# Kernel tuning notes

Hardware: AMD Instinct MI355X
Metric: run time of the kernel (lower is better)

## Reference

```python
import jax, jax.numpy as jnp
import numpy as np

N_NODES = 100000
N_EDGES = 1600000
D = 64
HID = 512
N_CLASSES = 393


def gcn_conv(x, src, dst, W, b):
    """PyG-style GCNConv: h = x W; add self-loops; symmetric deg^-1/2 norm; scatter-add."""
    n = x.shape[0]
    h = x @ W  # [N, out]
    loop = jnp.arange(n)
    s = jnp.concatenate([src, loop])
    d = jnp.concatenate([dst, loop])
    deg = jax.ops.segment_sum(jnp.ones(d.shape[0], dtype=h.dtype), d, num_segments=n)
    dinv = jax.lax.rsqrt(jnp.maximum(deg, 1.0))  # self-loops guarantee deg >= 1
    norm = dinv[s] * dinv[d]  # [E+N]
    msg = h[s] * norm[:, None]  # [E+N, out] gather + scale
    out = jax.ops.segment_sum(msg, d, num_segments=n)  # scatter-add
    return out + b


def setup_inputs() -> dict:
    key = jax.random.key(0)
    ks = jax.random.split(key, 10)
    sc = 1.0 / np.sqrt(D)
    inp = {
        "adj": jax.random.randint(ks[0], (2, N_EDGES), 0, N_NODES, dtype=jnp.int64),
        "features": jax.random.normal(ks[1], (N_NODES, D), dtype=jnp.float32),
        "W1": jax.random.normal(ks[2], (D, D), dtype=jnp.float32) * sc,
        "b1": jnp.zeros((D,), jnp.float32),
        "W2": jax.random.normal(ks[3], (D, D), dtype=jnp.float32) * sc,
        "b2": jnp.zeros((D,), jnp.float32),
        "W3": jax.random.normal(ks[4], (D, D), dtype=jnp.float32) * sc,
        "b3": jnp.zeros((D,), jnp.float32),
        "Wlin": jax.random.normal(ks[5], (D, D), dtype=jnp.float32) * sc,
        "blin": jnp.zeros((D,), jnp.float32),
        "W4": jax.random.normal(ks[6], (N_NODES, HID), dtype=jnp.float32) / np.sqrt(N_NODES),
        "b4": jnp.zeros((HID,), jnp.float32),
        "W5": jax.random.normal(ks[7], (HID, N_CLASSES), dtype=jnp.float32) / np.sqrt(HID),
        "b5": jnp.zeros((N_CLASSES,), jnp.float32),
    }
    return inp


def reference(adj, features, W1, b1, W2, b2, W3, b3, Wlin, blin, W4, b4, W5, b5):
    src, dst = adj[0], adj[1]
    h = jax.nn.relu(gcn_conv(features, src, dst, W1, b1))
    h = jax.nn.relu(gcn_conv(h, src, dst, W2, b2))
    h = jax.nn.relu(gcn_conv(h, src, dst, W3, b3))
    scores = h @ Wlin + blin          # [N, 64]
    scores = scores.T                 # [64, N]
    scores = jax.nn.relu(scores @ W4 + b4)  # [64, HID]
    scores = scores @ W5 + b5         # [64, n_classes]
    return jax.nn.log_softmax(scores, axis=1)
```

## Files before the change

kernel.cpp:

```cpp
#include <hip/hip_runtime.h>
#include <math.h>

#define NN 100000
#define NE 1600000
#define HID 512
#define NCLS 393

__global__ void k_init(int* __restrict__ cnt, int* __restrict__ gtot) {
    int i = blockIdx.x * 256 + threadIdx.x;
    if (i < NN) cnt[i] = 0;
    if (i == 0) *gtot = 0;
}

__global__ void k_count(const int* __restrict__ dst, int* __restrict__ cnt) {
    int e = blockIdx.x * 256 + threadIdx.x;
    if (e < NE) atomicAdd(&cnt[dst[e]], 1);
}

__global__ void k_off(const int* __restrict__ cnt, float* __restrict__ dinv,
                      int* __restrict__ off, int* __restrict__ cur, int* __restrict__ gtot) {
    int i = blockIdx.x * 256 + threadIdx.x;
    if (i < NN) {
        int c = cnt[i];
        dinv[i] = rsqrtf(1.0f + (float)c);
        off[i] = atomicAdd(gtot, c);
        cur[i] = 0;
    }
}

__global__ void k_fill(const int* __restrict__ src, const int* __restrict__ dst,
                       const float* __restrict__ dinv, const int* __restrict__ off,
                       int* __restrict__ cur, int2* __restrict__ epack) {
    int e = blockIdx.x * 256 + threadIdx.x;
    if (e < NE) {
        int s = src[e], d = dst[e];
        int pos = off[d] + atomicAdd(&cur[d], 1);
        epack[pos] = make_int2(s, __float_as_int(dinv[s] * dinv[d]));
    }
}

template<bool IN_ACT, bool OUT_BIAS>
__global__ void k_gemm64b(const float* __restrict__ x, const float* __restrict__ W,
                          const float* __restrict__ bin, const float* __restrict__ bout,
                          float* __restrict__ out) {
    __shared__ float Ws[64 * 64];
    __shared__ float xs[32 * 64];
    int tid = threadIdx.x;
    size_t n0 = (size_t)blockIdx.x * 32;
    for (int i = tid; i < 1024; i += 256)
        ((float4*)Ws)[i] = ((const float4*)W)[i];
    for (int i = tid; i < 512; i += 256) {
        float4 v = ((const float4*)(x + n0 * 64))[i];
        if (IN_ACT) {
            int c = (i & 15) * 4;
            float4 bv = *(const float4*)(bin + c);
            v.x = fmaxf(v.x + bv.x, 0.f);
            v.y = fmaxf(v.y + bv.y, 0.f);
            v.z = fmaxf(v.z + bv.z, 0.f);
            v.w = fmaxf(v.w + bv.w, 0.f);
        }
        ((float4*)xs)[i] = v;
    }
    __syncthreads();
    int j = tid & 63, q = tid >> 6;
    float Wreg[64];
#pragma unroll
    for (int k = 0; k < 64; ++k) Wreg[k] = Ws[k * 64 + j];
    float bo = OUT_BIAS ? bout[j] : 0.f;
    for (int r = 0; r < 8; ++r) {
        int row = q * 8 + r;
        float acc = bo;
        const float4* xr = (const float4*)(xs + row * 64);
#pragma unroll
        for (int k4 = 0; k4 < 16; ++k4) {
            float4 xv = xr[k4];
            acc = fmaf(xv.x, Wreg[k4 * 4 + 0], acc);
            acc = fmaf(xv.y, Wreg[k4 * 4 + 1], acc);
            acc = fmaf(xv.z, Wreg[k4 * 4 + 2], acc);
            acc = fmaf(xv.w, Wreg[k4 * 4 + 3], acc);
        }
        out[(n0 + row) * 64 + j] = acc;
    }
}

__global__ void k_gather2(const int2* __restrict__ epack, const int* __restrict__ off,
                          const int* __restrict__ cnt, const float* __restrict__ dinv,
                          const float* __restrict__ t, float* __restrict__ out) {
    int lane = threadIdx.x & 63;
    int n = (blockIdx.x * 256 + threadIdx.x) >> 6;
    if (n >= NN) return;
    int g = lane >> 4, f4 = lane & 15;
    int o = off[n], c = cnt[n];
    float ax = 0.f, ay = 0.f, az = 0.f, aw = 0.f;
    for (int b = 0; b < c; b += 4) {
        int idx = b + g;
        if (idx < c) {
            int2 ep = epack[o + idx];
            float w = __int_as_float(ep.y);
            float4 v = *(const float4*)(t + (size_t)ep.x * 64 + f4 * 4);
            ax = fmaf(v.x, w, ax);
            ay = fmaf(v.y, w, ay);
            az = fmaf(v.z, w, az);
            aw = fmaf(v.w, w, aw);
        }
    }
    ax += __shfl_xor(ax, 16); ay += __shfl_xor(ay, 16);
    az += __shfl_xor(az, 16); aw += __shfl_xor(aw, 16);
    ax += __shfl_xor(ax, 32); ay += __shfl_xor(ay, 32);
    az += __shfl_xor(az, 32); aw += __shfl_xor(aw, 32);
    if (lane < 16) {
        float dv = dinv[n];
        float d2 = dv * dv;
        float4 self = *(const float4*)(t + (size_t)n * 64 + f4 * 4);
        float4 r;
        r.x = ax + self.x * d2;
        r.y = ay + self.y * d2;
        r.z = az + self.z * d2;
        r.w = aw + self.w * d2;
        *(float4*)(out + (size_t)n * 64 + f4 * 4) = r;
    }
}

#define TG_SPLIT 192
#define TG_CHUNK 521
__global__ void k_tgemm3(const float* __restrict__ scores, const float* __restrict__ W4,
                         float* __restrict__ Pp) {
    __shared__ float ss[64 * 64];
    int colT = blockIdx.x & 3;
    int kc = blockIdx.x >> 2;
    int tid = threadIdx.x;
    int tc = tid & 31, tr = tid >> 5;
    int col = colT * 128 + tc * 4;
    float acc[8][4];
#pragma unroll
    for (int i = 0; i < 8; ++i)
#pragma unroll
        for (int c = 0; c < 4; ++c) acc[i][c] = 0.f;
    int k0 = kc * TG_CHUNK;
    int k1 = min(k0 + TG_CHUNK, NN);
    for (int kb = k0; kb < k1; kb += 64) {
        int cnt = min(64, k1 - kb);
        __syncthreads();
        for (int i = tid; i < 1024; i += 256) {
            float4 v = {0.f, 0.f, 0.f, 0.f};
            if ((i >> 4) < cnt) v = ((const float4*)(scores + (size_t)kb * 64))[i];
            ((float4*)ss)[i] = v;
        }
        __syncthreads();
        const float* w4base = W4 + (size_t)kb * 512 + col;
        for (int nIt = 0; nIt < cnt; ++nIt) {
            float4 w = *(const float4*)(w4base + (size_t)nIt * 512);
            const float4* sp = (const float4*)(ss + nIt * 64 + tr * 8);
            float4 s0 = sp[0], s1 = sp[1];
            float sa[8] = {s0.x, s0.y, s0.z, s0.w, s1.x, s1.y, s1.z, s1.w};
#pragma unroll
            for (int i = 0; i < 8; ++i) {
                acc[i][0] = fmaf(sa[i], w.x, acc[i][0]);
                acc[i][1] = fmaf(sa[i], w.y, acc[i][1]);
                acc[i][2] = fmaf(sa[i], w.z, acc[i][2]);
                acc[i][3] = fmaf(sa[i], w.w, acc[i][3]);
            }
        }
    }
    float* pb = Pp + (size_t)kc * 64 * 512;
#pragma unroll
    for (int i = 0; i < 8; ++i) {
        int row = tr * 8 + i;
        *(float4*)(pb + row * 512 + col) = make_float4(acc[i][0], acc[i][1], acc[i][2], acc[i][3]);
    }
}

__global__ void k_reduce(const float* __restrict__ Pp, float* __restrict__ P) {
    int i = blockIdx.x * 256 + threadIdx.x;
    float s0 = 0.f, s1 = 0.f, s2 = 0.f, s3 = 0.f;
    for (int kc = 0; kc < TG_SPLIT; kc += 4) {
        s0 += Pp[(size_t)(kc + 0) * 32768 + i];
        s1 += Pp[(size_t)(kc + 1) * 32768 + i];
        s2 += Pp[(size_t)(kc + 2) * 32768 + i];
        s3 += Pp[(size_t)(kc + 3) * 32768 + i];
    }
    P[i] = (s0 + s1) + (s2 + s3);
}

__global__ void k_final(const float* __restrict__ P, const float* __restrict__ b4,
                        const float* __restrict__ W5, const float* __restrict__ b5,
                        float* __restrict__ out) {
    __shared__ float p[HID];
    __shared__ float z[NCLS];
    __shared__ float red[256];
    int i = blockIdx.x;
    int tid = threadIdx.x;
    for (int k = tid; k < HID; k += 256) p[k] = fmaxf(P[i * HID + k] + b4[k], 0.f);
    __syncthreads();
    for (int c = tid; c < NCLS; c += 256) {
        float acc = b5[c];
        for (int k = 0; k < HID; ++k) acc = fmaf(p[k], W5[(size_t)k * NCLS + c], acc);
        z[c] = acc;
    }
    __syncthreads();
    float m = -INFINITY;
    for (int c = tid; c < NCLS; c += 256) m = fmaxf(m, z[c]);
    red[tid] = m;
    __syncthreads();
    for (int s = 128; s > 0; s >>= 1) {
        if (tid < s) red[tid] = fmaxf(red[tid], red[tid + s]);
        __syncthreads();
    }
    m = red[0];
    __syncthreads();
    float sum = 0.f;
    for (int c = tid; c < NCLS; c += 256) sum += expf(z[c] - m);
    red[tid] = sum;
    __syncthreads();
    for (int s = 128; s > 0; s >>= 1) {
        if (tid < s) red[tid] += red[tid + s];
        __syncthreads();
    }
    float lse = m + logf(red[0]);
    for (int c = tid; c < NCLS; c += 256) out[i * NCLS + c] = z[c] - lse;
}

extern "C" void kernel_launch(void* const* d_in, const int* in_sizes, int n_in,
                              void* d_out, int out_size, void* d_ws, size_t ws_size,
                              hipStream_t stream) {
    const int* adj = (const int*)d_in[0];
    const int* src = adj;
    const int* dst = adj + NE;
    const float* feat = (const float*)d_in[1];
    const float* W1 = (const float*)d_in[2];
    const float* b1 = (const float*)d_in[3];
    const float* W2 = (const float*)d_in[4];
    const float* b2 = (const float*)d_in[5];
    const float* W3 = (const float*)d_in[6];
    const float* b3 = (const float*)d_in[7];
    const float* Wlin = (const float*)d_in[8];
    const float* blin = (const float*)d_in[9];
    const float* W4 = (const float*)d_in[10];
    const float* b4 = (const float*)d_in[11];
    const float* W5 = (const float*)d_in[12];
    const float* b5 = (const float*)d_in[13];
    float* out = (float*)d_out;

    char* ws = (char*)d_ws;
    float* dinv  = (float*)ws;  ws += (size_t)NN * 4;
    int*   cnt   = (int*)ws;    ws += (size_t)NN * 4;
    int*   off   = (int*)ws;    ws += (size_t)NN * 4;
    int*   cur   = (int*)ws;    ws += (size_t)NN * 4;
    int*   gtot  = (int*)ws;    ws += 16;
    int2*  epack = (int2*)ws;   ws += (size_t)NE * 8;
    float* bufA  = (float*)ws;  ws += (size_t)NN * 64 * 4;
    float* bufB  = (float*)ws;  ws += (size_t)NN * 64 * 4;
    float* P     = (float*)ws;  ws += 64 * HID * 4;

    const int NB_N = (NN + 255) / 256;
    const int NB_E = NE / 256;
    const int NB_G = NN / 32;
    const int NB_GA = NN / 4;
    const int NB_T = 4 * TG_SPLIT;

    k_init<<<NB_N, 256, 0, stream>>>(cnt, gtot);
    k_count<<<NB_E, 256, 0, stream>>>(dst, cnt);
    k_off<<<NB_N, 256, 0, stream>>>(cnt, dinv, off, cur, gtot);
    k_fill<<<NB_E, 256, 0, stream>>>(src, dst, dinv, off, cur, epack);

    k_gemm64b<false, false><<<NB_G, 256, 0, stream>>>(feat, W1, nullptr, nullptr, bufA);
    k_gather2<<<NB_GA, 256, 0, stream>>>(epack, off, cnt, dinv, bufA, bufB);
    k_gemm64b<true, false><<<NB_G, 256, 0, stream>>>(bufB, W2, b1, nullptr, bufA);
    k_gather2<<<NB_GA, 256, 0, stream>>>(epack, off, cnt, dinv, bufA, bufB);
    k_gemm64b<true, false><<<NB_G, 256, 0, stream>>>(bufB, W3, b2, nullptr, bufA);
    k_gather2<<<NB_GA, 256, 0, stream>>>(epack, off, cnt, dinv, bufA, bufB);
    k_gemm64b<true, true><<<NB_G, 256, 0, stream>>>(bufB, Wlin, b3, blin, bufA);

    float* Pp = bufB;
    k_tgemm3<<<NB_T, 256, 0, stream>>>(bufA, W4, Pp);
    k_reduce<<<(64 * HID) / 256, 256, 0, stream>>>(Pp, P);

    k_final<<<64, 256, 0, stream>>>(P, b4, W5, b5, out);
}
```

Measured before the change: 958.9 us.

## Widen gather per-lane loads, rebalance tgemm split, and replace init with memset

The neighbor gather now processes 8 edges per step, with each lane loading 8 floats. It clamps indices instead of branching, so more row loads are in flight per wavefront. The big transposed GEMM uses more, shorter K chunks with fixed trip counts and batches four W4 row loads ahead. The partial sums are reduced by a block-level 4-way split. Smaller changes swap the init kernel for hipMemsetAsync, give the 64x64 GEMM two accumulators, and reorder the workspace so the larger partial buffer may overwrite the dead edge list.

```diff
diff --git a/kernel.cpp b/kernel.cpp
--- a/kernel.cpp
+++ b/kernel.cpp
@@ -5,12 +5,6 @@
 #define NE 1600000
 #define HID 512
 #define NCLS 393
-
-__global__ void k_init(int* __restrict__ cnt, int* __restrict__ gtot) {
-    int i = blockIdx.x * 256 + threadIdx.x;
-    if (i < NN) cnt[i] = 0;
-    if (i == 0) *gtot = 0;
-}
 
 __global__ void k_count(const int* __restrict__ dst, int* __restrict__ cnt) {
     int e = blockIdx.x * 256 + threadIdx.x;
@@ -69,61 +63,78 @@
     float bo = OUT_BIAS ? bout[j] : 0.f;
     for (int r = 0; r < 8; ++r) {
         int row = q * 8 + r;
-        float acc = bo;
+        float accA = bo, accB = 0.f;
         const float4* xr = (const float4*)(xs + row * 64);
 #pragma unroll
-        for (int k4 = 0; k4 < 16; ++k4) {
-            float4 xv = xr[k4];
-            acc = fmaf(xv.x, Wreg[k4 * 4 + 0], acc);
-            acc = fmaf(xv.y, Wreg[k4 * 4 + 1], acc);
-            acc = fmaf(xv.z, Wreg[k4 * 4 + 2], acc);
-            acc = fmaf(xv.w, Wreg[k4 * 4 + 3], acc);
-        }
-        out[(n0 + row) * 64 + j] = acc;
-    }
-}
-
-__global__ void k_gather2(const int2* __restrict__ epack, const int* __restrict__ off,
+        for (int k4 = 0; k4 < 16; k4 += 2) {
+            float4 x0 = xr[k4], x1 = xr[k4 + 1];
+            accA = fmaf(x0.x, Wreg[k4 * 4 + 0], accA);
+            accA = fmaf(x0.y, Wreg[k4 * 4 + 1], accA);
+            accA = fmaf(x0.z, Wreg[k4 * 4 + 2], accA);
+            accA = fmaf(x0.w, Wreg[k4 * 4 + 3], accA);
+            accB = fmaf(x1.x, Wreg[k4 * 4 + 4], accB);
+            accB = fmaf(x1.y, Wreg[k4 * 4 + 5], accB);
+            accB = fmaf(x1.z, Wreg[k4 * 4 + 6], accB);
+            accB = fmaf(x1.w, Wreg[k4 * 4 + 7], accB);
+        }
+        out[(n0 + row) * 64 + j] = accA + accB;
+    }
+}
+
+__global__ void k_gather3(const int2* __restrict__ epack, const int* __restrict__ off,
                           const int* __restrict__ cnt, const float* __restrict__ dinv,
                           const float* __restrict__ t, float* __restrict__ out) {
     int lane = threadIdx.x & 63;
     int n = (blockIdx.x * 256 + threadIdx.x) >> 6;
     if (n >= NN) return;
-    int g = lane >> 4, f4 = lane & 15;
+    int g = lane >> 3, fl = lane & 7;
     int o = off[n], c = cnt[n];
-    float ax = 0.f, ay = 0.f, az = 0.f, aw = 0.f;
-    for (int b = 0; b < c; b += 4) {
-        int idx = b + g;
-        if (idx < c) {
-            int2 ep = epack[o + idx];
-            float w = __int_as_float(ep.y);
-            float4 v = *(const float4*)(t + (size_t)ep.x * 64 + f4 * 4);
-            ax = fmaf(v.x, w, ax);
-            ay = fmaf(v.y, w, ay);
-            az = fmaf(v.z, w, az);
-            aw = fmaf(v.w, w, aw);
-        }
-    }
-    ax += __shfl_xor(ax, 16); ay += __shfl_xor(ay, 16);
-    az += __shfl_xor(az, 16); aw += __shfl_xor(aw, 16);
-    ax += __shfl_xor(ax, 32); ay += __shfl_xor(ay, 32);
-    az += __shfl_xor(az, 32); aw += __shfl_xor(aw, 32);
-    if (lane < 16) {
+    float4 a0 = {0.f, 0.f, 0.f, 0.f}, a1 = {0.f, 0.f, 0.f, 0.f};
+    if (c > 0) {
+        for (int b = 0; b < c; b += 8) {
+            int idx = b + g;
+            int2 ep = epack[o + min(idx, c - 1)];
+            float w = (idx < c) ? __int_as_float(ep.y) : 0.f;
+            const float* row = t + (size_t)ep.x * 64 + fl * 8;
+            float4 v0 = *(const float4*)row;
+            float4 v1 = *(const float4*)(row + 4);
+            a0.x = fmaf(v0.x, w, a0.x);
+            a0.y = fmaf(v0.y, w, a0.y);
+            a0.z = fmaf(v0.z, w, a0.z);
+            a0.w = fmaf(v0.w, w, a0.w);
+            a1.x = fmaf(v1.x, w, a1.x);
+            a1.y = fmaf(v1.y, w, a1.y);
+            a1.z = fmaf(v1.z, w, a1.z);
+            a1.w = fmaf(v1.w, w, a1.w);
+        }
+    }
+#pragma unroll
+    for (int m = 8; m <= 32; m <<= 1) {
+        a0.x += __shfl_xor(a0.x, m); a0.y += __shfl_xor(a0.y, m);
+        a0.z += __shfl_xor(a0.z, m); a0.w += __shfl_xor(a0.w, m);
+        a1.x += __shfl_xor(a1.x, m); a1.y += __shfl_xor(a1.y, m);
+        a1.z += __shfl_xor(a1.z, m); a1.w += __shfl_xor(a1.w, m);
+    }
+    if (lane < 8) {
         float dv = dinv[n];
         float d2 = dv * dv;
-        float4 self = *(const float4*)(t + (size_t)n * 64 + f4 * 4);
-        float4 r;
-        r.x = ax + self.x * d2;
-        r.y = ay + self.y * d2;
-        r.z = az + self.z * d2;
-        r.w = aw + self.w * d2;
-        *(float4*)(out + (size_t)n * 64 + f4 * 4) = r;
-    }
-}
-
-#define TG_SPLIT 192
-#define TG_CHUNK 521
-__global__ void k_tgemm3(const float* __restrict__ scores, const float* __restrict__ W4,
+        const float* srow = t + (size_t)n * 64 + fl * 8;
+        float4 s0 = *(const float4*)srow;
+        float4 s1 = *(const float4*)(srow + 4);
+        float4 r0, r1;
+        r0.x = a0.x + s0.x * d2; r0.y = a0.y + s0.y * d2;
+        r0.z = a0.z + s0.z * d2; r0.w = a0.w + s0.w * d2;
+        r1.x = a1.x + s1.x * d2; r1.y = a1.y + s1.y * d2;
+        r1.z = a1.z + s1.z * d2; r1.w = a1.w + s1.w * d2;
+        float* orow = out + (size_t)n * 64 + fl * 8;
+        *(float4*)orow = r0;
+        *(float4*)(orow + 4) = r1;
+    }
+}
+
+#define TG_SPLIT 261
+#define TG_CHUNK 384
+__global__ void k_tgemm4(const float* __restrict__ scores, const float* __restrict__ W4,
                          float* __restrict__ Pp) {
     __shared__ float ss[64 * 64];
     int colT = blockIdx.x & 3;
@@ -137,28 +148,34 @@
 #pragma unroll
         for (int c = 0; c < 4; ++c) acc[i][c] = 0.f;
     int k0 = kc * TG_CHUNK;
-    int k1 = min(k0 + TG_CHUNK, NN);
-    for (int kb = k0; kb < k1; kb += 64) {
-        int cnt = min(64, k1 - kb);
+    for (int st = 0; st < 6; ++st) {
+        int kb = k0 + st * 64;
         __syncthreads();
         for (int i = tid; i < 1024; i += 256) {
             float4 v = {0.f, 0.f, 0.f, 0.f};
-            if ((i >> 4) < cnt) v = ((const float4*)(scores + (size_t)kb * 64))[i];
+            if (kb + (i >> 4) < NN) v = ((const float4*)(scores + (size_t)kb * 64))[i];
             ((float4*)ss)[i] = v;
         }
         __syncthreads();
-        const float* w4base = W4 + (size_t)kb * 512 + col;
-        for (int nIt = 0; nIt < cnt; ++nIt) {
-            float4 w = *(const float4*)(w4base + (size_t)nIt * 512);
-            const float4* sp = (const float4*)(ss + nIt * 64 + tr * 8);
-            float4 s0 = sp[0], s1 = sp[1];
-            float sa[8] = {s0.x, s0.y, s0.z, s0.w, s1.x, s1.y, s1.z, s1.w};
-#pragma unroll
-            for (int i = 0; i < 8; ++i) {
-                acc[i][0] = fmaf(sa[i], w.x, acc[i][0]);
-                acc[i][1] = fmaf(sa[i], w.y, acc[i][1]);
-                acc[i][2] = fmaf(sa[i], w.z, acc[i][2]);
-                acc[i][3] = fmaf(sa[i], w.w, acc[i][3]);
+        for (int nIt = 0; nIt < 64; nIt += 4) {
+            float4 w[4];
+#pragma unroll
+            for (int u = 0; u < 4; ++u) {
+                int row = min(kb + nIt + u, NN - 1);
+                w[u] = *(const float4*)(W4 + (size_t)row * 512 + col);
+            }
+#pragma unroll
+            for (int u = 0; u < 4; ++u) {
+                const float4* sp = (const float4*)(ss + (nIt + u) * 64 + tr * 8);
+                float4 s0 = sp[0], s1 = sp[1];
+                float sa[8] = {s0.x, s0.y, s0.z, s0.w, s1.x, s1.y, s1.z, s1.w};
+#pragma unroll
+                for (int i = 0; i < 8; ++i) {
+                    acc[i][0] = fmaf(sa[i], w[u].x, acc[i][0]);
+                    acc[i][1] = fmaf(sa[i], w[u].y, acc[i][1]);
+                    acc[i][2] = fmaf(sa[i], w[u].z, acc[i][2]);
+                    acc[i][3] = fmaf(sa[i], w[u].w, acc[i][3]);
+                }
             }
         }
     }
@@ -170,16 +187,17 @@
     }
 }
 
-__global__ void k_reduce(const float* __restrict__ Pp, float* __restrict__ P) {
-    int i = blockIdx.x * 256 + threadIdx.x;
-    float s0 = 0.f, s1 = 0.f, s2 = 0.f, s3 = 0.f;
-    for (int kc = 0; kc < TG_SPLIT; kc += 4) {
-        s0 += Pp[(size_t)(kc + 0) * 32768 + i];
-        s1 += Pp[(size_t)(kc + 1) * 32768 + i];
-        s2 += Pp[(size_t)(kc + 2) * 32768 + i];
-        s3 += Pp[(size_t)(kc + 3) * 32768 + i];
-    }
-    P[i] = (s0 + s1) + (s2 + s3);
+__global__ void k_reduce2(const float* __restrict__ Pp, float* __restrict__ P) {
+    __shared__ float red[256];
+    int tid = threadIdx.x;
+    int o = blockIdx.x * 64 + (tid & 63);
+    int q = tid >> 6;
+    int k0 = q * 66, k1 = min(k0 + 66, TG_SPLIT);
+    float s = 0.f;
+    for (int kc = k0; kc < k1; ++kc) s += Pp[(size_t)kc * 32768 + o];
+    red[tid] = s;
+    __syncthreads();
+    if (tid < 64) P[o] = red[tid] + red[tid + 64] + red[tid + 128] + red[tid + 192];
 }
 
 __global__ void k_final(const float* __restrict__ P, const float* __restrict__ b4,
@@ -242,14 +260,14 @@
     float* out = (float*)d_out;
 
     char* ws = (char*)d_ws;
+    int*   cnt   = (int*)ws;    ws += (size_t)NN * 4;
+    int*   gtot  = (int*)ws;    ws += 16;
     float* dinv  = (float*)ws;  ws += (size_t)NN * 4;
-    int*   cnt   = (int*)ws;    ws += (size_t)NN * 4;
     int*   off   = (int*)ws;    ws += (size_t)NN * 4;
     int*   cur   = (int*)ws;    ws += (size_t)NN * 4;
-    int*   gtot  = (int*)ws;    ws += 16;
-    int2*  epack = (int2*)ws;   ws += (size_t)NE * 8;
     float* bufA  = (float*)ws;  ws += (size_t)NN * 64 * 4;
     float* bufB  = (float*)ws;  ws += (size_t)NN * 64 * 4;
+    int2*  epack = (int2*)ws;   ws += (size_t)NE * 8;
     float* P     = (float*)ws;  ws += 64 * HID * 4;
 
     const int NB_N = (NN + 255) / 256;
@@ -258,22 +276,22 @@
     const int NB_GA = NN / 4;
     const int NB_T = 4 * TG_SPLIT;
 
-    k_init<<<NB_N, 256, 0, stream>>>(cnt, gtot);
+    hipMemsetAsync(cnt, 0, (size_t)NN * 4 + 16, stream);
     k_count<<<NB_E, 256, 0, stream>>>(dst, cnt);
     k_off<<<NB_N, 256, 0, stream>>>(cnt, dinv, off, cur, gtot);
     k_fill<<<NB_E, 256, 0, stream>>>(src, dst, dinv, off, cur, epack);
 
     k_gemm64b<false, false><<<NB_G, 256, 0, stream>>>(feat, W1, nullptr, nullptr, bufA);
-    k_gather2<<<NB_GA, 256, 0, stream>>>(epack, off, cnt, dinv, bufA, bufB);
+    k_gather3<<<NB_GA, 256, 0, stream>>>(epack, off, cnt, dinv, bufA, bufB);
     k_gemm64b<true, false><<<NB_G, 256, 0, stream>>>(bufB, W2, b1, nullptr, bufA);
-    k_gather2<<<NB_GA, 256, 0, stream>>>(epack, off, cnt, dinv, bufA, bufB);
+    k_gather3<<<NB_GA, 256, 0, stream>>>(epack, off, cnt, dinv, bufA, bufB);
     k_gemm64b<true, false><<<NB_G, 256, 0, stream>>>(bufB, W3, b2, nullptr, bufA);
-    k_gather2<<<NB_GA, 256, 0, stream>>>(epack, off, cnt, dinv, bufA, bufB);
+    k_gather3<<<NB_GA, 256, 0, stream>>>(epack, off, cnt, dinv, bufA, bufB);
     k_gemm64b<true, true><<<NB_G, 256, 0, stream>>>(bufB, Wlin, b3, blin, bufA);
 
     float* Pp = bufB;
-    k_tgemm3<<<NB_T, 256, 0, stream>>>(bufA, W4, Pp);
-    k_reduce<<<(64 * HID) / 256, 256, 0, stream>>>(Pp, P);
+    k_tgemm4<<<NB_T, 256, 0, stream>>>(bufA, W4, Pp);
+    k_reduce2<<<512, 256, 0, stream>>>(Pp, P);
 
     k_final<<<64, 256, 0, stream>>>(P, b4, W5, b5, out);
 }
```

Result: slower. 984.9 us (+2.7%).
